# Kernel tuning notes

Hardware: AMD Instinct MI355X
Metric: run time of the kernel (lower is better)

Reference implementation:

```python
import jax, jax.numpy as jnp
import numpy as np

N_NODES = 50000
N_EDGES = 600000
D_NODE_IN = 32
D_EDGE_IN = 16
H = 128
D_OUT = 2
N_PASSES = 5
LN_EPS = 1e-6  # flax LayerNorm default


def _dense(key, fan_in, fan_out, scale=0.05):
    return (jax.random.normal(key, (fan_in, fan_out), dtype=jnp.float32) * scale)


def setup_inputs() -> dict:
    key = jax.random.key(0)
    ks = jax.random.split(key, 16)
    inp = {
        "nodes": jax.random.normal(ks[0], (N_NODES, D_NODE_IN), dtype=jnp.float32),
        "edges": jax.random.normal(ks[1], (N_EDGES, D_EDGE_IN), dtype=jnp.float32),
        "senders": jax.random.randint(ks[2], (N_EDGES,), 0, N_NODES, dtype=jnp.int32),
        "receivers": jax.random.randint(ks[3], (N_EDGES,), 0, N_NODES, dtype=jnp.int32),
        # node encoder ReluMLP [128,128]
        "enc_n_W0": _dense(ks[4], D_NODE_IN, H), "enc_n_b0": jnp.zeros((H,), jnp.float32),
        "enc_n_W1": _dense(ks[5], H, H), "enc_n_b1": jnp.zeros((H,), jnp.float32),
        # edge encoder ReluMLP [128,128]
        "enc_e_W0": _dense(ks[6], D_EDGE_IN, H), "enc_e_b0": jnp.zeros((H,), jnp.float32),
        "enc_e_W1": _dense(ks[7], H, H), "enc_e_b1": jnp.zeros((H,), jnp.float32),
        # weight-tied LinearMessagePassingLayer params
        "W_msg": _dense(ks[8], H + H, H),                 # Dense(no bias) on concat(sender_feat, edge)
        "node_W0": _dense(ks[9], H + H, H), "node_b0": jnp.zeros((H,), jnp.float32),
        "node_W1": _dense(ks[10], H, H), "node_b1": jnp.zeros((H,), jnp.float32),
        "W_node": _dense(ks[11], H, H),                   # residual projection, no bias
        "ln_g": jnp.ones((H,), jnp.float32), "ln_b": jnp.zeros((H,), jnp.float32),
        # node decoder ReluMLP [128,2]
        "dec_W0": _dense(ks[12], H, H), "dec_b0": jnp.zeros((H,), jnp.float32),
        "dec_W1": _dense(ks[13], H, D_OUT), "dec_b1": jnp.zeros((D_OUT,), jnp.float32),
    }
    return inp


def _relu_mlp(x, layers):
    # Dense+ReLU for all but last layer; last layer linear.
    n = len(layers)
    for i, (W, b) in enumerate(layers):
        x = x @ W + b
        if i < n - 1:
            x = jax.nn.relu(x)
    return x


def _layer_norm(x, g, b):
    mu = jnp.mean(x, axis=-1, keepdims=True)
    var = jnp.var(x, axis=-1, keepdims=True)
    return (x - mu) * jax.lax.rsqrt(var + LN_EPS) * g + b


def reference(nodes, edges, senders, receivers,
              enc_n_W0, enc_n_b0, enc_n_W1, enc_n_b1,
              enc_e_W0, enc_e_b0, enc_e_W1, enc_e_b1,
              W_msg, node_W0, node_b0, node_W1, node_b1,
              W_node, ln_g, ln_b,
              dec_W0, dec_b0, dec_W1, dec_b1):
    n = _relu_mlp(nodes, [(enc_n_W0, enc_n_b0), (enc_n_W1, enc_n_b1)])  # [N,H]
    e = _relu_mlp(edges, [(enc_e_W0, enc_e_b0), (enc_e_W1, enc_e_b1)])  # [E,H]
    total_nodes = n.shape[0]

    for _ in range(N_PASSES):  # weight-tied process block
        sender_features = n[senders]                                    # gather [E,H]
        msg_in = jnp.concatenate([sender_features, e], axis=-1)         # [E,2H]
        messages = msg_in @ W_msg                                       # [E,H]
        agg = jax.ops.segment_sum(messages, receivers, num_segments=total_nodes)
        node_in = jnp.concatenate([n, agg], axis=-1)                    # [N,2H]
        nodes_out = _relu_mlp(node_in, [(node_W0, node_b0), (node_W1, node_b1)])
        n = _layer_norm(n @ W_node + nodes_out, ln_g, ln_b)

    return _relu_mlp(n, [(dec_W0, dec_b0), (dec_W1, dec_b1)])           # [N,2]
```

## Files before the change

### kernel.cpp

```cpp
#include <hip/hip_runtime.h>

#define DEVFN __device__ __forceinline__

namespace {

constexpr int NN = 50000;
constexpr int NE = 600000;
constexpr int H  = 128;
constexpr float LN_EPS = 1e-6f;

typedef _Float16 f16x8 __attribute__((ext_vector_type(8)));
typedef _Float16 f16x4 __attribute__((ext_vector_type(4)));
typedef float f32x4 __attribute__((ext_vector_type(4)));

DEVFN void mm_block(const float* xsrow, int pitch, int K,
                    const float* __restrict__ W, int c0, float (&acc)[8][4]) {
  for (int k = 0; k < K; k += 4) {
    float4 w0 = *(const float4*)(W + (size_t)(k + 0) * H + c0);
    float4 w1 = *(const float4*)(W + (size_t)(k + 1) * H + c0);
    float4 w2 = *(const float4*)(W + (size_t)(k + 2) * H + c0);
    float4 w3 = *(const float4*)(W + (size_t)(k + 3) * H + c0);
#pragma unroll
    for (int r = 0; r < 8; ++r) {
      float4 a = *(const float4*)(xsrow + r * pitch + k);
      acc[r][0] += a.x * w0.x; acc[r][0] += a.y * w1.x; acc[r][0] += a.z * w2.x; acc[r][0] += a.w * w3.x;
      acc[r][1] += a.x * w0.y; acc[r][1] += a.y * w1.y; acc[r][1] += a.z * w2.y; acc[r][1] += a.w * w3.y;
      acc[r][2] += a.x * w0.z; acc[r][2] += a.y * w1.z; acc[r][2] += a.z * w2.z; acc[r][2] += a.w * w3.z;
      acc[r][3] += a.x * w0.w; acc[r][3] += a.y * w1.w; acc[r][3] += a.z * w2.w; acc[r][3] += a.w * w3.w;
    }
  }
}

DEVFN void linear_body(const float* __restrict__ x, const float* __restrict__ W,
                       float* __restrict__ y, int r0, int R, int t, float* xs) {
  {
    const int r = t & 31, q = t >> 5;
    int row = r0 + r;
    if (row >= R) row = R - 1;
    const float* src = &x[(size_t)row * H + q * 32];
#pragma unroll
    for (int j = 0; j < 8; ++j)
      *(float4*)&xs[r * 132 + q * 32 + j * 4] = *(const float4*)&src[j * 4];
  }
  __syncthreads();
  const int c0 = (t & 31) * 4;
  const int rbase = (t >> 5) * 8;
  float acc[8][4];
#pragma unroll
  for (int r = 0; r < 8; ++r) { acc[r][0] = 0.f; acc[r][1] = 0.f; acc[r][2] = 0.f; acc[r][3] = 0.f; }
  mm_block(&xs[rbase * 132], 132, H, W, c0, acc);
#pragma unroll
  for (int r = 0; r < 8; ++r) {
    int row = r0 + rbase + r;
    if (row < R)
      *(float4*)&y[(size_t)row * H + c0] =
          make_float4(acc[r][0], acc[r][1], acc[r][2], acc[r][3]);
  }
}

__global__ __launch_bounds__(128) void fold1_kernel(
    const float* __restrict__ Wb, const float* __restrict__ Wt,
    const float* __restrict__ W0b, float* __restrict__ T,
    float* __restrict__ Wf) {
  __shared__ float xs[32 * 132];
  const float* x = (blockIdx.x < 4) ? Wb : Wt;
  float* y = (blockIdx.x < 4) ? T : Wf;
  linear_body(x, W0b, y, (blockIdx.x & 3) * 32, 128, threadIdx.x, xs);
}

__global__ __launch_bounds__(128) void fold2_kernel(
    const float* __restrict__ W1e, const float* __restrict__ b1e,
    const float* __restrict__ T, float* __restrict__ Wc2,
    float* __restrict__ bc2) {
  __shared__ float xs[32 * 132];
  if (blockIdx.x < 4) {
    linear_body(W1e, T, Wc2, blockIdx.x * 32, 128, threadIdx.x, xs);
  } else {
    int j = threadIdx.x;
    float s = 0.f;
    for (int k = 0; k < H; ++k) s += b1e[k] * T[(size_t)k * H + j];
    bc2[j] = s;
  }
}

__global__ __launch_bounds__(64) void prepack7_kernel(
    const float* __restrict__ s0, const float* __restrict__ s1,
    const float* __restrict__ s2, const float* __restrict__ s3,
    const float* __restrict__ s4, const float* __restrict__ s5,
    const float* __restrict__ s6, _Float16* __restrict__ pkBase) {
  const int z = blockIdx.z;
  const float* W = (z == 0) ? s0 : (z == 1) ? s1 : (z == 2) ? s2 :
                   (z == 3) ? s3 : (z == 4) ? s4 : (z == 5) ? s5 : s6;
  _Float16* pk = pkBase + (size_t)z * 128 * H;
  const int ks = blockIdx.x, ct = blockIdx.y, l = threadIdx.x;
  const int kbase = ks * 32 + (l >> 4) * 8;
  const int col = ct * 16 + (l & 15);
  _Float16 tmp[8];
#pragma unroll
  for (int j = 0; j < 8; ++j)
    tmp[j] = (_Float16)W[(size_t)(kbase + j) * H + col];
  *(f16x8*)&pk[((size_t)((ks * 8 + ct) * 64) + l) * 8] = *(f16x8*)tmp;
}

__global__ __launch_bounds__(64) void prepack_w0e_kernel(
    const float* __restrict__ W0e, const float* __restrict__ b0e,
    _Float16* __restrict__ pk) {
  const int ct = blockIdx.x, l = threadIdx.x;
  const int quad = l >> 4;
  const int col = ct * 16 + (l & 15);
  _Float16 tmp[8];
#pragma unroll
  for (int j = 0; j < 8; ++j) {
    int k = quad * 8 + j;
    float v = (quad < 2) ? W0e[(size_t)k * H + col] : (k == 16 ? b0e[col] : 0.f);
    tmp[j] = (_Float16)v;
  }
  *(f16x8*)&pk[((size_t)(ct * 64) + l) * 8] = *(f16x8*)tmp;
}

__global__ __launch_bounds__(64) void prepack_k32_kernel(
    const float* __restrict__ W, _Float16* __restrict__ pk) {
  const int ct = blockIdx.x, l = threadIdx.x;
  const int quad = l >> 4;
  const int col = ct * 16 + (l & 15);
  _Float16 tmp[8];
#pragma unroll
  for (int j = 0; j < 8; ++j)
    tmp[j] = (_Float16)W[(size_t)(quad * 8 + j) * H + col];
  *(f16x8*)&pk[((size_t)(ct * 64) + l) * 8] = *(f16x8*)tmp;
}

__global__ __launch_bounds__(256) void hist_kernel(const int* __restrict__ recv,
                                                   int* __restrict__ cnt) {
  int i = blockIdx.x * 256 + threadIdx.x;
  if (i < NE) atomicAdd(&cnt[recv[i]], 1);
}

__global__ __launch_bounds__(256) void scan1_kernel(const int* __restrict__ cnt,
                                                    int* __restrict__ excl,
                                                    int* __restrict__ part) {
  __shared__ int s[256];
  int t = threadIdx.x;
  int i = blockIdx.x * 256 + t;
  int v = (i < NN) ? cnt[i] : 0;
  s[t] = v;
  __syncthreads();
  for (int off = 1; off < 256; off <<= 1) {
    int x = (t >= off) ? s[t - off] : 0;
    __syncthreads();
    s[t] += x;
    __syncthreads();
  }
  if (i < NN) excl[i] = s[t] - v;
  if (t == 255) part[blockIdx.x] = s[255];
}

__global__ __launch_bounds__(256) void scan2_kernel(int* __restrict__ part, int nb) {
  __shared__ int s[256];
  int t = threadIdx.x;
  int v = (t < nb) ? part[t] : 0;
  s[t] = v;
  __syncthreads();
  for (int off = 1; off < 256; off <<= 1) {
    int x = (t >= off) ? s[t - off] : 0;
    __syncthreads();
    s[t] += x;
    __syncthreads();
  }
  if (t < nb) part[t] = s[t] - v;
}

__global__ __launch_bounds__(256) void scan3_kernel(int* __restrict__ excl,
                                                    const int* __restrict__ part,
                                                    int* __restrict__ cursor) {
  int i = blockIdx.x * 256 + threadIdx.x;
  if (i < NN) {
    int e = excl[i] + part[i >> 8];
    excl[i] = e;
    cursor[i] = e;
  }
}

__global__ __launch_bounds__(256) void scatter_permute_kernel(
    const int* __restrict__ senders, const int* __restrict__ recv,
    int* __restrict__ cursor, const float* __restrict__ edges,
    int* __restrict__ sendp, _Float16* __restrict__ edgesP16) {
  const int t = threadIdx.x;
  const int i = blockIdx.x * 64 + (t >> 2);
  if (i >= NE) return;
  const int sub = t & 3;
  int pos = 0;
  if (sub == 0) pos = atomicAdd(&cursor[recv[i]], 1);
  pos = __shfl(pos, (t & 63) & ~3);
  if (sub == 0) sendp[pos] = senders[i];
  float4 v = *(const float4*)&edges[(size_t)i * 16 + sub * 4];
  f16x4 h = {(_Float16)v.x, (_Float16)v.y, (_Float16)v.z, (_Float16)v.w};
  *(f16x4*)&edgesP16[(size_t)pos * 16 + sub * 4] = h;
}

__global__ __launch_bounds__(256) void encoder_mfma_kernel(
    const float* __restrict__ x, const float* __restrict__ b0,
    const float* __restrict__ b1, const _Float16* __restrict__ pkEW0,
    const _Float16* __restrict__ pkEW1, _Float16* __restrict__ outp) {
  __shared__ _Float16 lds[4][16 * 136];
  const int t = threadIdx.x;
  const int wave = t >> 6, lane = t & 63;
  const int row0 = blockIdx.x * 64 + wave * 16;
  const int quad = lane >> 4, m16 = lane & 15;
  _Float16* hlds = &lds[wave][0];

  int arow = row0 + m16;
  if (arow >= NN) arow = NN - 1;
  f16x8 a0;
  {
    const float* src = &x[(size_t)arow * 32 + quad * 8];
    float4 v0 = *(const float4*)(src);
    float4 v1 = *(const float4*)(src + 4);
    a0[0] = (_Float16)v0.x; a0[1] = (_Float16)v0.y;
    a0[2] = (_Float16)v0.z; a0[3] = (_Float16)v0.w;
    a0[4] = (_Float16)v1.x; a0[5] = (_Float16)v1.y;
    a0[6] = (_Float16)v1.z; a0[7] = (_Float16)v1.w;
  }
#pragma unroll
  for (int ct = 0; ct < 8; ++ct) {
    float bb = b0[ct * 16 + m16];
    f32x4 acc = (f32x4){bb, bb, bb, bb};
    acc = __builtin_amdgcn_mfma_f32_16x16x32_f16(
        a0, *(const f16x8*)&pkEW0[((size_t)(ct * 64) + lane) * 8], acc, 0, 0, 0);
#pragma unroll
    for (int q = 0; q < 4; ++q)
      hlds[(quad * 4 + q) * 136 + ct * 16 + m16] = (_Float16)fmaxf(acc[q], 0.f);
  }
  __syncthreads();
  const _Float16* hrow = &hlds[m16 * 136 + quad * 8];
  f16x8 ah[4];
#pragma unroll
  for (int ks = 0; ks < 4; ++ks) ah[ks] = *(const f16x8*)(hrow + ks * 32);
  f32x4 acc2[8];
#pragma unroll
  for (int ct = 0; ct < 8; ++ct) {
    float bb = b1[ct * 16 + m16];
    acc2[ct] = (f32x4){bb, bb, bb, bb};
  }
#pragma unroll
  for (int ks = 0; ks < 4; ++ks) {
    const _Float16* bp = pkEW1 + ((size_t)ks * 8 * 64 + lane) * 8;
#pragma unroll
    for (int ct = 0; ct < 8; ++ct)
      acc2[ct] = __builtin_amdgcn_mfma_f32_16x16x32_f16(
          ah[ks], *(const f16x8*)(bp + ct * 512), acc2[ct], 0, 0, 0);
  }
  __syncthreads();
#pragma unroll
  for (int ct = 0; ct < 8; ++ct)
#pragma unroll
    for (int q = 0; q < 4; ++q)
      hlds[(quad * 4 + q) * 136 + ct * 16 + m16] = (_Float16)acc2[ct][q];
  __syncthreads();
  {
    int lr = lane >> 2, cc = (lane & 3) * 32;
    int orow = row0 + lr;
    if (orow < NN) {
      const _Float16* src = &hlds[lr * 136 + cc];
      _Float16* dst = &outp[(size_t)orow * H + cc];
      *(f16x8*)(dst + 0)  = *(const f16x8*)(src + 0);
      *(f16x8*)(dst + 8)  = *(const f16x8*)(src + 8);
      *(f16x8*)(dst + 16) = *(const f16x8*)(src + 16);
      *(f16x8*)(dst + 24) = *(const f16x8*)(src + 24);
    }
  }
}

__global__ __launch_bounds__(256) void hsblin_kernel(
    const _Float16* __restrict__ edgesP16, const int* __restrict__ start,
    const int* __restrict__ endc, const _Float16* __restrict__ pkW0e,
    const _Float16* __restrict__ pkWc2, const float* __restrict__ bc2,
    _Float16* __restrict__ B2pk) {
  __shared__ _Float16 hl[16][136];
  __shared__ float degl[16];
  const int t = threadIdx.x;
  const int wave = t >> 6, lane = t & 63;
  const int quad = lane >> 4, m16 = lane & 15;
  const int tile = blockIdx.x;
  const int vb = tile * 16 + wave * 4;

  f16x8 bfrag[8];
#pragma unroll
  for (int ct = 0; ct < 8; ++ct)
    bfrag[ct] = *(const f16x8*)&pkW0e[((size_t)(ct * 64) + lane) * 8];

  int j0[4], dg[4];
#pragma unroll
  for (int k = 0; k < 4; ++k) j0[k] = start[vb + k];
#pragma unroll
  for (int k = 0; k < 4; ++k) dg[k] = endc[vb + k] - j0[k];

  float rs[4][8];
#pragma unroll
  for (int k = 0; k < 4; ++k)
#pragma unroll
    for (int ct = 0; ct < 8; ++ct) rs[k][ct] = 0.f;

  f16x8 a0[4];
#pragma unroll
  for (int k = 0; k < 4; ++k) {
    const bool valid = (m16 < dg[k]);
    f16x8 a = {};
    if (quad < 2) {
      if (valid)
        a = *(const f16x8*)&edgesP16[(size_t)(j0[k] + m16) * 16 + quad * 8];
    } else if (quad == 2) {
      a[0] = valid ? (_Float16)1.f : (_Float16)0.f;
    }
    a0[k] = a;
  }
#pragma unroll
  for (int k = 0; k < 4; ++k) {
#pragma unroll
    for (int ct = 0; ct < 8; ++ct) {
      f32x4 acc = (f32x4){0.f, 0.f, 0.f, 0.f};
      acc = __builtin_amdgcn_mfma_f32_16x16x32_f16(a0[k], bfrag[ct], acc, 0, 0, 0);
      rs[k][ct] += (fmaxf(acc[0], 0.f) + fmaxf(acc[1], 0.f)) +
                   (fmaxf(acc[2], 0.f) + fmaxf(acc[3], 0.f));
    }
  }
#pragma unroll
  for (int k = 0; k < 4; ++k) {
    for (int base = 16; base < dg[k]; base += 16) {
      const bool valid = (base + m16 < dg[k]);
      f16x8 a = {};
      if (quad < 2) {
        if (valid)
          a = *(const f16x8*)&edgesP16[(size_t)(j0[k] + base + m16) * 16 + quad * 8];
      } else if (quad == 2) {
        a[0] = valid ? (_Float16)1.f : (_Float16)0.f;
      }
#pragma unroll
      for (int ct = 0; ct < 8; ++ct) {
        f32x4 acc = (f32x4){0.f, 0.f, 0.f, 0.f};
        acc = __builtin_amdgcn_mfma_f32_16x16x32_f16(a, bfrag[ct], acc, 0, 0, 0);
        rs[k][ct] += (fmaxf(acc[0], 0.f) + fmaxf(acc[1], 0.f)) +
                     (fmaxf(acc[2], 0.f) + fmaxf(acc[3], 0.f));
      }
    }
  }
#pragma unroll
  for (int k = 0; k < 4; ++k) {
#pragma unroll
    for (int ct = 0; ct < 8; ++ct) {
      float s = rs[k][ct];
      s += __shfl_xor(s, 16);
      s += __shfl_xor(s, 32);
      rs[k][ct] = s;
    }
    const int nl = wave * 4 + k;
    if (lane < 16) {
#pragma unroll
      for (int ct = 0; ct < 8; ++ct)
        hl[nl][ct * 16 + lane] = (_Float16)rs[k][ct];
    }
    if (lane == 16) degl[nl] = (float)dg[k];
  }
  __syncthreads();

  f16x8 ah[4];
#pragma unroll
  for (int ks = 0; ks < 4; ++ks)
    ah[ks] = *(const f16x8*)&hl[m16][ks * 32 + quad * 8];
  float degq[4];
#pragma unroll
  for (int q = 0; q < 4; ++q) degq[q] = degl[quad * 4 + q];
  f32x4 acc2[2];
#pragma unroll
  for (int i = 0; i < 2; ++i) {
    int ct = wave * 2 + i;
    float bcv = bc2[ct * 16 + m16];
    acc2[i] = (f32x4){degq[0] * bcv, degq[1] * bcv, degq[2] * bcv, degq[3] * bcv};
  }
#pragma unroll
  for (int ks = 0; ks < 4; ++ks) {
#pragma unroll
    for (int i = 0; i < 2; ++i) {
      int ct = wave * 2 + i;
      const _Float16* bp = pkWc2 + ((size_t)((ks * 8 + ct) * 64) + lane) * 8;
      acc2[i] = __builtin_amdgcn_mfma_f32_16x16x32_f16(
          ah[ks], *(const f16x8*)bp, acc2[i], 0, 0, 0);
    }
  }
  _Float16 tmp[8];
#pragma unroll
  for (int i = 0; i < 2; ++i)
#pragma unroll
    for (int q = 0; q < 4; ++q) tmp[i * 4 + q] = (_Float16)acc2[i][q];
  *(f16x8*)&B2pk[((size_t)tile * 64 + lane) * 32 + wave * 8] = *(f16x8*)tmp;
}

__global__ __launch_bounds__(256) void gather_kernel(
    const _Float16* __restrict__ n16, const int* __restrict__ start,
    const int* __restrict__ endc, const int* __restrict__ sendp,
    _Float16* __restrict__ S) {
  const int t = threadIdx.x;
  const int v = blockIdx.x * 4 + (t >> 6);
  const int lane = t & 63;
  const int grp = lane >> 4;
  const int c = (lane & 15) * 8;
  float a[8] = {0.f, 0.f, 0.f, 0.f, 0.f, 0.f, 0.f, 0.f};
  const int e = endc[v];
  int j = start[v];
  for (; j + 7 < e; j += 8) {
    int s0 = sendp[j + grp];
    int s1 = sendp[j + 4 + grp];
    f16x8 p0 = *(const f16x8*)&n16[(size_t)s0 * H + c];
    f16x8 p1 = *(const f16x8*)&n16[(size_t)s1 * H + c];
#pragma unroll
    for (int i = 0; i < 8; ++i) a[i] += (float)p0[i] + (float)p1[i];
  }
  for (; j < e; j += 4) {
    int jj = j + grp;
    if (jj < e) {
      int s0 = sendp[jj];
      f16x8 p0 = *(const f16x8*)&n16[(size_t)s0 * H + c];
#pragma unroll
      for (int i = 0; i < 8; ++i) a[i] += (float)p0[i];
    }
  }
#pragma unroll
  for (int i = 0; i < 8; ++i) {
    a[i] += __shfl_xor(a[i], 16);
    a[i] += __shfl_xor(a[i], 32);
  }
  if (lane < 16) {
    f16x8 o;
#pragma unroll
    for (int i = 0; i < 8; ++i) o[i] = (_Float16)a[i];
    *(f16x8*)&S[(size_t)v * H + c] = o;
  }
}

__global__ __launch_bounds__(256) void node_mfma_kernel(
    const _Float16* __restrict__ n16, const _Float16* __restrict__ S16,
    const _Float16* __restrict__ B2pk,
    const _Float16* __restrict__ pkW0t, const _Float16* __restrict__ pkWf,
    const float* __restrict__ b0,
    const _Float16* __restrict__ pkW1, const _Float16* __restrict__ pkWn,
    const float* __restrict__ b1,
    const float* __restrict__ ln_g, const float* __restrict__ ln_b,
    _Float16* __restrict__ nout) {
  __shared__ _Float16 lds[4][16 * 136];
  const int t = threadIdx.x;
  const int wave = t >> 6, lane = t & 63;
  const int row0 = blockIdx.x * 64 + wave * 16;
  const int quad = lane >> 4, m16 = lane & 15;
  _Float16* hlds = &lds[wave][0];

  int arow = row0 + m16;
  if (arow >= NN) arow = NN - 1;
  const _Float16* nrow = &n16[(size_t)arow * H + quad * 8];
  const _Float16* srow = &S16[(size_t)arow * H + quad * 8];
  f16x8 an[4], as[4];
#pragma unroll
  for (int ks = 0; ks < 4; ++ks) {
    an[ks] = *(const f16x8*)(nrow + ks * 32);
    as[ks] = *(const f16x8*)(srow + ks * 32);
  }

  const int tile = blockIdx.x * 4 + wave;
  const _Float16* b2l = &B2pk[((size_t)tile * 64 + lane) * 32];
  f32x4 acc[8];
#pragma unroll
  for (int ct = 0; ct < 8; ++ct) {
    float bb = b0[ct * 16 + m16];
    f16x4 bv = *(const f16x4*)(b2l + ct * 4);
    acc[ct] = (f32x4){bb + (float)bv[0], bb + (float)bv[1],
                      bb + (float)bv[2], bb + (float)bv[3]};
  }
#pragma unroll
  for (int ks = 0; ks < 4; ++ks) {
    const _Float16* bp0 = pkW0t + ((size_t)ks * 8 * 64 + lane) * 8;
    const _Float16* bpf = pkWf + ((size_t)ks * 8 * 64 + lane) * 8;
#pragma unroll
    for (int ct = 0; ct < 8; ++ct) {
      f16x8 bw0 = *(const f16x8*)(bp0 + ct * 512);
      acc[ct] = __builtin_amdgcn_mfma_f32_16x16x32_f16(an[ks], bw0, acc[ct], 0, 0, 0);
      f16x8 bwf = *(const f16x8*)(bpf + ct * 512);
      acc[ct] = __builtin_amdgcn_mfma_f32_16x16x32_f16(as[ks], bwf, acc[ct], 0, 0, 0);
    }
  }
#pragma unroll
  for (int ct = 0; ct < 8; ++ct) {
#pragma unroll
    for (int q = 0; q < 4; ++q)
      hlds[(quad * 4 + q) * 136 + ct * 16 + m16] =
          (_Float16)fmaxf(acc[ct][q], 0.f);
  }
  __syncthreads();

  const _Float16* hrow = &hlds[m16 * 136 + quad * 8];
  f32x4 acc2[8];
#pragma unroll
  for (int ct = 0; ct < 8; ++ct) {
    float bb = b1[ct * 16 + m16];
    acc2[ct] = (f32x4){bb, bb, bb, bb};
  }
#pragma unroll
  for (int ks = 0; ks < 4; ++ks) {
    f16x8 ah = *(const f16x8*)(hrow + ks * 32);
    const _Float16* bp1 = pkW1 + ((size_t)ks * 8 * 64 + lane) * 8;
    const _Float16* bpn = pkWn + ((size_t)ks * 8 * 64 + lane) * 8;
#pragma unroll
    for (int ct = 0; ct < 8; ++ct) {
      f16x8 b1f = *(const f16x8*)(bp1 + ct * 512);
      acc2[ct] = __builtin_amdgcn_mfma_f32_16x16x32_f16(ah, b1f, acc2[ct], 0, 0, 0);
      f16x8 bnf = *(const f16x8*)(bpn + ct * 512);
      acc2[ct] = __builtin_amdgcn_mfma_f32_16x16x32_f16(an[ks], bnf, acc2[ct], 0, 0, 0);
    }
  }

  float gv[8], bv[8];
#pragma unroll
  for (int ct = 0; ct < 8; ++ct) {
    gv[ct] = ln_g[ct * 16 + m16];
    bv[ct] = ln_b[ct * 16 + m16];
  }
  __syncthreads();
#pragma unroll
  for (int q = 0; q < 4; ++q) {
    float s1 = 0.f, s2 = 0.f;
#pragma unroll
    for (int ct = 0; ct < 8; ++ct) {
      float v = acc2[ct][q];
      s1 += v; s2 += v * v;
    }
#pragma unroll
    for (int m = 1; m <= 8; m <<= 1) {
      s1 += __shfl_xor(s1, m);
      s2 += __shfl_xor(s2, m);
    }
    float mu = s1 * (1.f / 128.f);
    float var = s2 * (1.f / 128.f) - mu * mu;
    float rs = rsqrtf(var + LN_EPS);
#pragma unroll
    for (int ct = 0; ct < 8; ++ct) {
      float o = (acc2[ct][q] - mu) * rs * gv[ct] + bv[ct];
      hlds[(quad * 4 + q) * 136 + ct * 16 + m16] = (_Float16)o;
    }
  }
  __syncthreads();

  {
    int lr = lane >> 2;
    int cc = (lane & 3) * 32;
    const _Float16* src = &hlds[lr * 136 + cc];
    int orow = row0 + lr;
    if (orow < NN) {
      _Float16* dst = &nout[(size_t)orow * H + cc];
      *(f16x8*)(dst + 0)  = *(const f16x8*)(src + 0);
      *(f16x8*)(dst + 8)  = *(const f16x8*)(src + 8);
      *(f16x8*)(dst + 16) = *(const f16x8*)(src + 16);
      *(f16x8*)(dst + 24) = *(const f16x8*)(src + 24);
    }
  }
}

__global__ __launch_bounds__(256) void decode_mfma_kernel(
    const _Float16* __restrict__ n, const float* __restrict__ b0,
    const _Float16* __restrict__ pkDW0, const float* __restrict__ W1,
    const float* __restrict__ b1, float* __restrict__ out) {
  const int t = threadIdx.x;
  const int wave = t >> 6, lane = t & 63;
  const int row0 = blockIdx.x * 64 + wave * 16;
  const int quad = lane >> 4, m16 = lane & 15;
  int arow = row0 + m16;
  if (arow >= NN) arow = NN - 1;
  const _Float16* nrow = &n[(size_t)arow * H + quad * 8];
  f16x8 an[4];
#pragma unroll
  for (int ks = 0; ks < 4; ++ks) an[ks] = *(const f16x8*)(nrow + ks * 32);
  f32x4 acc[8];
#pragma unroll
  for (int ct = 0; ct < 8; ++ct) {
    float bb = b0[ct * 16 + m16];
    acc[ct] = (f32x4){bb, bb, bb, bb};
  }
#pragma unroll
  for (int ks = 0; ks < 4; ++ks) {
    const _Float16* bp = pkDW0 + ((size_t)ks * 8 * 64 + lane) * 8;
#pragma unroll
    for (int ct = 0; ct < 8; ++ct)
      acc[ct] = __builtin_amdgcn_mfma_f32_16x16x32_f16(
          an[ks], *(const f16x8*)(bp + ct * 512), acc[ct], 0, 0, 0);
  }
  float s0[4] = {0.f, 0.f, 0.f, 0.f}, s1[4] = {0.f, 0.f, 0.f, 0.f};
#pragma unroll
  for (int ct = 0; ct < 8; ++ct) {
    const float2 w = *(const float2*)&W1[(size_t)(ct * 16 + m16) * 2];
#pragma unroll
    for (int q = 0; q < 4; ++q) {
      float h = fmaxf(acc[ct][q], 0.f);
      s0[q] += h * w.x;
      s1[q] += h * w.y;
    }
  }
#pragma unroll
  for (int q = 0; q < 4; ++q) {
#pragma unroll
    for (int m = 1; m <= 8; m <<= 1) {
      s0[q] += __shfl_xor(s0[q], m);
      s1[q] += __shfl_xor(s1[q], m);
    }
  }
  if (m16 == 0) {
#pragma unroll
    for (int q = 0; q < 4; ++q) {
      int r = row0 + quad * 4 + q;
      if (r < NN) {
        out[(size_t)r * 2 + 0] = s0[q] + b1[0];
        out[(size_t)r * 2 + 1] = s1[q] + b1[1];
      }
    }
  }
}

__global__ __launch_bounds__(256) void zero_kernel(float4* __restrict__ p, int n4) {
  int i = blockIdx.x * 256 + threadIdx.x;
  if (i < n4) p[i] = make_float4(0.f, 0.f, 0.f, 0.f);
}

}

extern "C" void kernel_launch(void* const* d_in, const int* in_sizes, int n_in,
                              void* d_out, int out_size, void* d_ws, size_t ws_size,
                              hipStream_t stream) {
  const float* nodes     = (const float*)d_in[0];
  const float* edges     = (const float*)d_in[1];
  const int*   senders   = (const int*)d_in[2];
  const int*   receivers = (const int*)d_in[3];
  const float* enc_n_W0 = (const float*)d_in[4];
  const float* enc_n_b0 = (const float*)d_in[5];
  const float* enc_n_W1 = (const float*)d_in[6];
  const float* enc_n_b1 = (const float*)d_in[7];
  const float* enc_e_W0 = (const float*)d_in[8];
  const float* enc_e_b0 = (const float*)d_in[9];
  const float* enc_e_W1 = (const float*)d_in[10];
  const float* enc_e_b1 = (const float*)d_in[11];
  const float* W_msg    = (const float*)d_in[12];
  const float* node_W0  = (const float*)d_in[13];
  const float* node_b0  = (const float*)d_in[14];
  const float* node_W1  = (const float*)d_in[15];
  const float* node_b1  = (const float*)d_in[16];
  const float* W_node   = (const float*)d_in[17];
  const float* ln_g     = (const float*)d_in[18];
  const float* ln_b     = (const float*)d_in[19];
  const float* dec_W0   = (const float*)d_in[20];
  const float* dec_b0   = (const float*)d_in[21];
  const float* dec_W1   = (const float*)d_in[22];
  const float* dec_b1   = (const float*)d_in[23];
  float* out = (float*)d_out;

  const float* Wt  = W_msg;
  const float* Wb  = W_msg + 128 * H;
  const float* W0t = node_W0;
  const float* W0b = node_W0 + 128 * H;

  const int mfmaBlocks = (NN + 63) / 64;
  const int nTiles     = mfmaBlocks * 4;
  const int hsTiles    = NN / 16;

  float* T      = (float*)d_ws;
  float* Wc2    = T + 128 * H;
  float* Wf32   = Wc2 + 128 * H;
  float* bc2    = Wf32 + 128 * H;
  _Float16* edgesP16 = (_Float16*)(bc2 + 128);
  _Float16* n16a  = edgesP16 + (size_t)NE * 16;
  _Float16* n16b  = n16a + (size_t)NN * H;
  _Float16* S16   = n16b + (size_t)NN * H;
  _Float16* B2pk  = S16 + (size_t)NN * H;
  _Float16* pkAll = B2pk + (size_t)nTiles * 64 * 32;
  _Float16* pkW0t = pkAll;
  _Float16* pkWf  = pkAll + 1 * 128 * H;
  _Float16* pkW1  = pkAll + 2 * 128 * H;
  _Float16* pkWn  = pkAll + 3 * 128 * H;
  _Float16* pkEW1 = pkAll + 4 * 128 * H;
  _Float16* pkDW0 = pkAll + 5 * 128 * H;
  _Float16* pkWc2 = pkAll + 6 * 128 * H;
  _Float16* pkW0e = pkAll + 7 * 128 * H;
  _Float16* pkEW0 = pkW0e + 4096;
  int* cnt    = (int*)(pkEW0 + 4096);
  int* excl   = cnt + NN;
  int* cursor = excl + NN;
  int* part   = cursor + NN;
  int* sendp  = part + 256;

  const int scanBlocks = (NN + 255) / 256;
  const int neBlocks   = (NE + 255) / 256;

  zero_kernel<<<(NN / 4 + 255) / 256, 256, 0, stream>>>((float4*)cnt, NN / 4);
  hist_kernel<<<neBlocks, 256, 0, stream>>>(receivers, cnt);
  scan1_kernel<<<scanBlocks, 256, 0, stream>>>(cnt, excl, part);
  scan2_kernel<<<1, 256, 0, stream>>>(part, scanBlocks);
  scan3_kernel<<<scanBlocks, 256, 0, stream>>>(excl, part, cursor);
  scatter_permute_kernel<<<(NE + 63) / 64, 256, 0, stream>>>(
      senders, receivers, cursor, edges, sendp, edgesP16);

  fold1_kernel<<<8, 128, 0, stream>>>(Wb, Wt, W0b, T, Wf32);
  fold2_kernel<<<5, 128, 0, stream>>>(enc_e_W1, enc_e_b1, T, Wc2, bc2);
  prepack7_kernel<<<dim3(4, 8, 7), 64, 0, stream>>>(
      W0t, Wf32, node_W1, W_node, enc_n_W1, dec_W0, Wc2, pkAll);
  prepack_w0e_kernel<<<8, 64, 0, stream>>>(enc_e_W0, enc_e_b0, pkW0e);
  prepack_k32_kernel<<<8, 64, 0, stream>>>(enc_n_W0, pkEW0);

  encoder_mfma_kernel<<<mfmaBlocks, 256, 0, stream>>>(
      nodes, enc_n_b0, enc_n_b1, pkEW0, pkEW1, n16a);
  zero_kernel<<<3, 256, 0, stream>>>(
      (float4*)(B2pk + (size_t)hsTiles * 64 * 32), (nTiles - hsTiles) * 512);
  hsblin_kernel<<<hsTiles, 256, 0, stream>>>(
      edgesP16, excl, cursor, pkW0e, pkWc2, bc2, B2pk);

  _Float16* ncur = n16a;
  _Float16* nnxt = n16b;
  for (int p = 0; p < 5; ++p) {
    gather_kernel<<<NN / 4, 256, 0, stream>>>(ncur, excl, cursor, sendp, S16);
    node_mfma_kernel<<<mfmaBlocks, 256, 0, stream>>>(
        ncur, S16, B2pk, pkW0t, pkWf, node_b0, pkW1, pkWn, node_b1,
        ln_g, ln_b, nnxt);
    _Float16* tmp = ncur; ncur = nnxt; nnxt = tmp;
  }

  decode_mfma_kernel<<<mfmaBlocks, 256, 0, stream>>>(
      ncur, dec_b0, pkDW0, dec_W1, dec_b1, out);
}
```

Before: 543.3 us.

## Fuse neighbor gather-sum into node MLP kernel via shared-memory staging

The separate per-node gather kernel is removed. Each node-MLP block now gathers and sums sender features for its 64 rows into shared memory: each 16-lane group handles four rows one after another, with four edges in flight per row. The MFMA stage then reads its aggregate operand from shared memory. This drops one launch per pass and the global write and read of the [N,H] aggregate buffer. In exchange, the latency-bound gather now runs in far fewer, larger blocks with a sequential loop over rows, which could reduce memory-level parallelism. Now-unneeded block barriers around the per-wave scratch buffer are also dropped.

New measurement: 747.2 us. +37.5%, slower.

```diff
diff --git a/kernel.cpp b/kernel.cpp
--- a/kernel.cpp
+++ b/kernel.cpp
@@ -395,50 +395,9 @@
   *(f16x8*)&B2pk[((size_t)tile * 64 + lane) * 32 + wave * 8] = *(f16x8*)tmp;
 }
 
-__global__ __launch_bounds__(256) void gather_kernel(
+__global__ __launch_bounds__(256) void node_fused_kernel(
     const _Float16* __restrict__ n16, const int* __restrict__ start,
     const int* __restrict__ endc, const int* __restrict__ sendp,
-    _Float16* __restrict__ S) {
-  const int t = threadIdx.x;
-  const int v = blockIdx.x * 4 + (t >> 6);
-  const int lane = t & 63;
-  const int grp = lane >> 4;
-  const int c = (lane & 15) * 8;
-  float a[8] = {0.f, 0.f, 0.f, 0.f, 0.f, 0.f, 0.f, 0.f};
-  const int e = endc[v];
-  int j = start[v];
-  for (; j + 7 < e; j += 8) {
-    int s0 = sendp[j + grp];
-    int s1 = sendp[j + 4 + grp];
-    f16x8 p0 = *(const f16x8*)&n16[(size_t)s0 * H + c];
-    f16x8 p1 = *(const f16x8*)&n16[(size_t)s1 * H + c];
-#pragma unroll
-    for (int i = 0; i < 8; ++i) a[i] += (float)p0[i] + (float)p1[i];
-  }
-  for (; j < e; j += 4) {
-    int jj = j + grp;
-    if (jj < e) {
-      int s0 = sendp[jj];
-      f16x8 p0 = *(const f16x8*)&n16[(size_t)s0 * H + c];
-#pragma unroll
-      for (int i = 0; i < 8; ++i) a[i] += (float)p0[i];
-    }
-  }
-#pragma unroll
-  for (int i = 0; i < 8; ++i) {
-    a[i] += __shfl_xor(a[i], 16);
-    a[i] += __shfl_xor(a[i], 32);
-  }
-  if (lane < 16) {
-    f16x8 o;
-#pragma unroll
-    for (int i = 0; i < 8; ++i) o[i] = (_Float16)a[i];
-    *(f16x8*)&S[(size_t)v * H + c] = o;
-  }
-}
-
-__global__ __launch_bounds__(256) void node_mfma_kernel(
-    const _Float16* __restrict__ n16, const _Float16* __restrict__ S16,
     const _Float16* __restrict__ B2pk,
     const _Float16* __restrict__ pkW0t, const _Float16* __restrict__ pkWf,
     const float* __restrict__ b0,
@@ -446,33 +405,71 @@
     const float* __restrict__ b1,
     const float* __restrict__ ln_g, const float* __restrict__ ln_b,
     _Float16* __restrict__ nout) {
-  __shared__ _Float16 lds[4][16 * 136];
+  __shared__ _Float16 sl[64 * 132];
+  __shared__ _Float16 hl[4][16 * 136];
   const int t = threadIdx.x;
   const int wave = t >> 6, lane = t & 63;
+  const int quad = lane >> 4, m16 = lane & 15;
   const int row0 = blockIdx.x * 64 + wave * 16;
-  const int quad = lane >> 4, m16 = lane & 15;
-  _Float16* hlds = &lds[wave][0];
 
   int arow = row0 + m16;
   if (arow >= NN) arow = NN - 1;
   const _Float16* nrow = &n16[(size_t)arow * H + quad * 8];
-  const _Float16* srow = &S16[(size_t)arow * H + quad * 8];
-  f16x8 an[4], as[4];
-#pragma unroll
-  for (int ks = 0; ks < 4; ++ks) {
-    an[ks] = *(const f16x8*)(nrow + ks * 32);
-    as[ks] = *(const f16x8*)(srow + ks * 32);
-  }
-
+  f16x8 an[4];
+#pragma unroll
+  for (int ks = 0; ks < 4; ++ks) an[ks] = *(const f16x8*)(nrow + ks * 32);
   const int tile = blockIdx.x * 4 + wave;
   const _Float16* b2l = &B2pk[((size_t)tile * 64 + lane) * 32];
+  f16x4 b2v[8];
+#pragma unroll
+  for (int ct = 0; ct < 8; ++ct) b2v[ct] = *(const f16x4*)(b2l + ct * 4);
+
+  {
+    const int g = t >> 4, gl = t & 15;
+    const _Float16* nb = n16 + gl * 8;
+#pragma unroll
+    for (int k = 0; k < 4; ++k) {
+      const int lr = g * 4 + k;
+      int row = blockIdx.x * 64 + lr;
+      if (row >= NN) row = NN - 1;
+      int j = start[row];
+      const int e = endc[row];
+      float a[8] = {0.f, 0.f, 0.f, 0.f, 0.f, 0.f, 0.f, 0.f};
+      for (; j + 3 < e; j += 4) {
+        int s0 = sendp[j], s1 = sendp[j + 1], s2 = sendp[j + 2], s3 = sendp[j + 3];
+        f16x8 p0 = *(const f16x8*)(nb + (size_t)s0 * H);
+        f16x8 p1 = *(const f16x8*)(nb + (size_t)s1 * H);
+        f16x8 p2 = *(const f16x8*)(nb + (size_t)s2 * H);
+        f16x8 p3 = *(const f16x8*)(nb + (size_t)s3 * H);
+#pragma unroll
+        for (int i = 0; i < 8; ++i)
+          a[i] += ((float)p0[i] + (float)p1[i]) + ((float)p2[i] + (float)p3[i]);
+      }
+      for (; j < e; ++j) {
+        int s0 = sendp[j];
+        f16x8 p0 = *(const f16x8*)(nb + (size_t)s0 * H);
+#pragma unroll
+        for (int i = 0; i < 8; ++i) a[i] += (float)p0[i];
+      }
+      f16x8 o;
+#pragma unroll
+      for (int i = 0; i < 8; ++i) o[i] = (_Float16)a[i];
+      *(f16x8*)&sl[lr * 132 + gl * 8] = o;
+    }
+  }
+  __syncthreads();
+
+  f16x8 as[4];
+#pragma unroll
+  for (int ks = 0; ks < 4; ++ks)
+    as[ks] = *(const f16x8*)&sl[(wave * 16 + m16) * 132 + ks * 32 + quad * 8];
+
   f32x4 acc[8];
 #pragma unroll
   for (int ct = 0; ct < 8; ++ct) {
     float bb = b0[ct * 16 + m16];
-    f16x4 bv = *(const f16x4*)(b2l + ct * 4);
-    acc[ct] = (f32x4){bb + (float)bv[0], bb + (float)bv[1],
-                      bb + (float)bv[2], bb + (float)bv[3]};
+    acc[ct] = (f32x4){bb + (float)b2v[ct][0], bb + (float)b2v[ct][1],
+                      bb + (float)b2v[ct][2], bb + (float)b2v[ct][3]};
   }
 #pragma unroll
   for (int ks = 0; ks < 4; ++ks) {
@@ -486,22 +483,19 @@
       acc[ct] = __builtin_amdgcn_mfma_f32_16x16x32_f16(as[ks], bwf, acc[ct], 0, 0, 0);
     }
   }
+  _Float16* h0 = &hl[wave][0];
 #pragma unroll
   for (int ct = 0; ct < 8; ++ct) {
 #pragma unroll
     for (int q = 0; q < 4; ++q)
-      hlds[(quad * 4 + q) * 136 + ct * 16 + m16] =
-          (_Float16)fmaxf(acc[ct][q], 0.f);
-  }
-  __syncthreads();
-
-  const _Float16* hrow = &hlds[m16 * 136 + quad * 8];
-  f32x4 acc2[8];
+      h0[(quad * 4 + q) * 136 + ct * 16 + m16] = (_Float16)fmaxf(acc[ct][q], 0.f);
+  }
 #pragma unroll
   for (int ct = 0; ct < 8; ++ct) {
     float bb = b1[ct * 16 + m16];
-    acc2[ct] = (f32x4){bb, bb, bb, bb};
-  }
+    acc[ct] = (f32x4){bb, bb, bb, bb};
+  }
+  const _Float16* hrow = &hl[wave][m16 * 136 + quad * 8];
 #pragma unroll
   for (int ks = 0; ks < 4; ++ks) {
     f16x8 ah = *(const f16x8*)(hrow + ks * 32);
@@ -510,9 +504,9 @@
 #pragma unroll
     for (int ct = 0; ct < 8; ++ct) {
       f16x8 b1f = *(const f16x8*)(bp1 + ct * 512);
-      acc2[ct] = __builtin_amdgcn_mfma_f32_16x16x32_f16(ah, b1f, acc2[ct], 0, 0, 0);
+      acc[ct] = __builtin_amdgcn_mfma_f32_16x16x32_f16(ah, b1f, acc[ct], 0, 0, 0);
       f16x8 bnf = *(const f16x8*)(bpn + ct * 512);
-      acc2[ct] = __builtin_amdgcn_mfma_f32_16x16x32_f16(an[ks], bnf, acc2[ct], 0, 0, 0);
+      acc[ct] = __builtin_amdgcn_mfma_f32_16x16x32_f16(an[ks], bnf, acc[ct], 0, 0, 0);
     }
   }
 
@@ -522,13 +516,12 @@
     gv[ct] = ln_g[ct * 16 + m16];
     bv[ct] = ln_b[ct * 16 + m16];
   }
-  __syncthreads();
 #pragma unroll
   for (int q = 0; q < 4; ++q) {
     float s1 = 0.f, s2 = 0.f;
 #pragma unroll
     for (int ct = 0; ct < 8; ++ct) {
-      float v = acc2[ct][q];
+      float v = acc[ct][q];
       s1 += v; s2 += v * v;
     }
 #pragma unroll
@@ -541,16 +534,14 @@
     float rs = rsqrtf(var + LN_EPS);
 #pragma unroll
     for (int ct = 0; ct < 8; ++ct) {
-      float o = (acc2[ct][q] - mu) * rs * gv[ct] + bv[ct];
-      hlds[(quad * 4 + q) * 136 + ct * 16 + m16] = (_Float16)o;
-    }
-  }
-  __syncthreads();
-
+      float o = (acc[ct][q] - mu) * rs * gv[ct] + bv[ct];
+      h0[(quad * 4 + q) * 136 + ct * 16 + m16] = (_Float16)o;
+    }
+  }
   {
     int lr = lane >> 2;
     int cc = (lane & 3) * 32;
-    const _Float16* src = &hlds[lr * 136 + cc];
+    const _Float16* src = &hl[wave][lr * 136 + cc];
     int orow = row0 + lr;
     if (orow < NN) {
       _Float16* dst = &nout[(size_t)orow * H + cc];
@@ -673,8 +664,7 @@
   _Float16* edgesP16 = (_Float16*)(bc2 + 128);
   _Float16* n16a  = edgesP16 + (size_t)NE * 16;
   _Float16* n16b  = n16a + (size_t)NN * H;
-  _Float16* S16   = n16b + (size_t)NN * H;
-  _Float16* B2pk  = S16 + (size_t)NN * H;
+  _Float16* B2pk  = n16b + (size_t)NN * H;
   _Float16* pkAll = B2pk + (size_t)nTiles * 64 * 32;
   _Float16* pkW0t = pkAll;
   _Float16* pkWf  = pkAll + 1 * 128 * H;
@@ -719,10 +709,9 @@
   _Float16* ncur = n16a;
   _Float16* nnxt = n16b;
   for (int p = 0; p < 5; ++p) {
-    gather_kernel<<<NN / 4, 256, 0, stream>>>(ncur, excl, cursor, sendp, S16);
-    node_mfma_kernel<<<mfmaBlocks, 256, 0, stream>>>(
-        ncur, S16, B2pk, pkW0t, pkWf, node_b0, pkW1, pkWn, node_b1,
-        ln_g, ln_b, nnxt);
+    node_fused_kernel<<<mfmaBlocks, 256, 0, stream>>>(
+        ncur, excl, cursor, sendp, B2pk, pkW0t, pkWf, node_b0,
+        pkW1, pkWn, node_b1, ln_g, ln_b, nnxt);
     _Float16* tmp = ncur; ncur = nnxt; nnxt = tmp;
   }
 
```
